# Performance work log

Hardware: AMD Instinct MI355X
Metric: run time of the kernel (lower is better)

## Reference

```python
import jax, jax.numpy as jnp
import numpy as np

GS = 128          # r_group_size
Q_MAX = 7.0       # 2**(q_bits-1)-1, q_bits=4
R_MAX = 7.0       # 2**(r_bits-1)-1, r_bits=4
R_MIN = -8.0      # -R_MAX-1
EPS = 1e-8


def _fake_quant_group(w, n_bits=4, group_size=128, eps=1e-8):
    # symmetric group-wise fake quant of the weight (done once at __init__)
    qmax = 2 ** (n_bits - 1) - 1
    qmin = -qmax - 1
    O, I = w.shape
    wg = w.reshape(O, I // group_size, group_size)
    scale = jnp.maximum(jnp.max(jnp.abs(wg), axis=-1, keepdims=True) / qmax, eps)
    wq = jnp.clip(jnp.round(wg / scale), qmin, qmax) * scale
    return wq.reshape(O, I)


def _select_pow2_base(t):
    # smallest value in {2,4,8,16,32,64} that is >= t (64 if none)
    base = jnp.full_like(t, 64.0)
    for v in (32.0, 16.0, 8.0, 4.0, 2.0):
        base = jnp.where(t <= v, jnp.full_like(t, v), base)
    return base


def setup_inputs() -> dict:
    key = jax.random.key(0)
    kx, kw, kb = jax.random.split(key, 3)
    B, S, IN, OUT = 4, 2048, 4096, 11008
    x = jax.random.normal(kx, (B, S, IN), dtype=jnp.float32)
    w_raw = jax.random.normal(kw, (OUT, IN), dtype=jnp.float32)
    weight = _fake_quant_group(w_raw, n_bits=4, group_size=128)
    bias = jax.random.normal(kb, (OUT,), dtype=jnp.float32)
    return {"x": x, "weight": weight, "bias": bias}


def reference(x, weight, bias):
    # dynamic quotient-remainder activation fake-quant (init path)
    H = x.shape[-1]
    xg = x.astype(jnp.float32).reshape(x.shape[:-1] + (H // GS, GS))  # [..., G, gs]
    max_abs = jnp.maximum(jnp.max(jnp.abs(xg), axis=-1, keepdims=True), EPS)
    base = _select_pow2_base(max_abs / Q_MAX)                 # [..., G, 1]
    q = jnp.clip(jnp.round(xg / base), -Q_MAX, Q_MAX)          # quotient
    r = xg - base * q                                          # remainder
    max_abs_r = jnp.maximum(jnp.max(jnp.abs(r), axis=-1, keepdims=True), EPS)
    scale_r = max_abs_r / R_MAX
    r_dq = jnp.clip(jnp.round(r / scale_r), R_MIN, R_MAX) * scale_r
    x_recon = (base * q + r_dq).reshape(x.shape)
    # F.linear: y = x @ W^T + b
    return jnp.einsum("bsi,oi->bso", x_recon, weight) + bias
```

## Files before the change

kernel.cpp:

```cpp
#include <hip/hip_runtime.h>
#include <stdint.h>
#include <stddef.h>

typedef __bf16 bf16x8 __attribute__((ext_vector_type(8)));
typedef float  f32x4  __attribute__((ext_vector_type(4)));
typedef float  f32x2  __attribute__((ext_vector_type(2)));

__device__ __forceinline__ unsigned short f2bf(float f) {
  unsigned int u = __builtin_bit_cast(unsigned int, f);
  u += 0x7fffu + ((u >> 16) & 1u);
  return (unsigned short)(u >> 16);
}

__device__ __forceinline__ void gld_lds16(const void* g, void* l) {
  __builtin_amdgcn_global_load_lds(
      (__attribute__((address_space(1))) void*)(g),
      (__attribute__((address_space(3))) void*)(l), 16, 0, 0);
}

#define BAR()     asm volatile("s_barrier" ::: "memory")
#define WAITVM(n) asm volatile("s_waitcnt vmcnt(" #n ")" ::: "memory")
#define SCHED0()  __builtin_amdgcn_sched_barrier(0)

__global__ __launch_bounds__(256) void quant_x_kernel(
    const float* __restrict__ x, unsigned short* __restrict__ xb, long long ngroups)
{
  const int lane = threadIdx.x & 63;
  const int wv   = threadIdx.x >> 6;
  long long g = (long long)blockIdx.x * 4 + wv;
  if (g >= ngroups) return;

  const float* xg = x + g * 128;
  f32x2 v = __builtin_nontemporal_load(
      reinterpret_cast<const f32x2*>(xg + lane * 2));

  float m = fmaxf(fabsf(v[0]), fabsf(v[1]));
  #pragma unroll
  for (int off = 32; off; off >>= 1) m = fmaxf(m, __shfl_xor(m, off));
  m = fmaxf(m, 1e-8f);

  float t = m / 7.0f;
  float base = t <= 2.f ? 2.f : t <= 4.f ? 4.f : t <= 8.f ? 8.f
             : t <= 16.f ? 16.f : t <= 32.f ? 32.f : 64.f;
  float inv_base = 1.0f / base;

  float q0 = fminf(fmaxf(rintf(v[0] * inv_base), -7.f), 7.f);
  float q1 = fminf(fmaxf(rintf(v[1] * inv_base), -7.f), 7.f);
  float r0 = v[0] - base * q0;
  float r1 = v[1] - base * q1;

  float mr = fmaxf(fabsf(r0), fabsf(r1));
  #pragma unroll
  for (int off = 32; off; off >>= 1) mr = fmaxf(mr, __shfl_xor(mr, off));
  mr = fmaxf(mr, 1e-8f);
  float scale_r = mr / 7.0f;

  float rd0 = fminf(fmaxf(rintf(r0 / scale_r), -8.f), 7.f) * scale_r;
  float rd1 = fminf(fmaxf(rintf(r1 / scale_r), -8.f), 7.f) * scale_r;

  float y0 = base * q0 + rd0;
  float y1 = base * q1 + rd1;

  unsigned int packed = (unsigned int)f2bf(y0) | ((unsigned int)f2bf(y1) << 16);
  *reinterpret_cast<unsigned int*>(xb + g * 128 + lane * 2) = packed;
}

__global__ __launch_bounds__(256) void cvt_w_kernel(
    const float* __restrict__ w, unsigned short* __restrict__ wb, long long n)
{
  long long i = ((long long)blockIdx.x * blockDim.x + threadIdx.x) * 8;
  if (i + 7 >= n) {
    if (i >= n) return;
    for (long long j = i; j < n; ++j) wb[j] = f2bf(w[j]);
    return;
  }
  f32x4 v0 = __builtin_nontemporal_load(reinterpret_cast<const f32x4*>(w + i));
  f32x4 v1 = __builtin_nontemporal_load(reinterpret_cast<const f32x4*>(w + i + 4));
  uint4 o;
  o.x = (unsigned)f2bf(v0[0]) | ((unsigned)f2bf(v0[1]) << 16);
  o.y = (unsigned)f2bf(v0[2]) | ((unsigned)f2bf(v0[3]) << 16);
  o.z = (unsigned)f2bf(v1[0]) | ((unsigned)f2bf(v1[1]) << 16);
  o.w = (unsigned)f2bf(v1[2]) | ((unsigned)f2bf(v1[3]) << 16);
  *reinterpret_cast<uint4*>(wb + i) = o;
}

#define BM 256
#define BN 256
#define BK 64

#define MFMA16(a, b, c) __builtin_amdgcn_mfma_f32_16x16x32_bf16(a, b, c, 0, 0, 0)

__global__ __launch_bounds__(512, 2) void gemm256_bias(
    const unsigned short* __restrict__ A,
    const unsigned short* __restrict__ B,
    const float* __restrict__ bias,
    float* __restrict__ C,
    int M, int N, int K)
{
  __shared__ unsigned short lds[2][2][2][128 * 64];

  const int tid  = threadIdx.x;
  const int lane = tid & 63;
  const int wid  = tid >> 6;
  const int wm   = wid >> 2;
  const int wn   = wid & 3;
  const int laneq = lane & 15;
  const int laneh = lane >> 4;
  const int lq7   = laneq & 7;

  const int ntm = M / BM;
  const int ntn = N / BN;
  int tm, tn;
  if ((ntm & 15) == 0) {
    int rem = blockIdx.x;
    int str = 0, stc = 0, w = 16;
    for (;;) {
      int w2 = (ntn - stc * 16 < 16) ? (ntn - stc * 16) : 16;
      int sz = 16 * w2;
      if (rem < sz) { w = w2; break; }
      rem -= sz;
      ++stc;
      if (stc * 16 >= ntn) { stc = 0; ++str; }
    }
    if (w == 16) {
      int x = rem & 7, q = rem >> 3;
      tm = str * 16 + 2 * (q & 7) + (x & 1);
      tn = stc * 16 + 4 * (q >> 3) + (x >> 1);
    } else {
      tm = str * 16 + rem / w;
      tn = stc * 16 + rem % w;
    }
  } else {
    tm = (int)blockIdx.x / ntn;
    tn = (int)blockIdx.x % ntn;
  }
  const size_t m0 = (size_t)tm * BM;
  const size_t n0 = (size_t)tn * BN;

  const int NT = K / BK;

  const int ss0 = (laneh ^ lq7);
  const int ss1 = ((4 + laneh) ^ lq7);

  const char* ldsb = (const char*)&lds[0][0][0][0];
  const int aOff = wm * 16384 + laneq * 128;
  const int bOff = 32768 + (wn >> 1) * 16384 + ((wn & 1) * 64 + laneq) * 128;

  const int c0 = tid, c1 = 512 + tid;
  const int r0 = c0 >> 3, sl0 = (c0 & 7) ^ (r0 & 7);
  const int r1 = c1 >> 3, sl1 = (c1 & 7) ^ (r1 & 7);
  const unsigned short* gA0 = A + (m0 + r0) * (size_t)K + sl0 * 8;
  const unsigned short* gA1 = A + (m0 + r1) * (size_t)K + sl1 * 8;
  const unsigned short* gB0 = B + (n0 + r0) * (size_t)K + sl0 * 8;
  const unsigned short* gB1 = B + (n0 + r1) * (size_t)K + sl1 * 8;
  const size_t hstep = (size_t)128 * K;

  char* dst0 = (char*)ldsb + wid * 1024;
  char* dst1 = dst0 + 65536;

  f32x4 acc[8][4];
  #pragma unroll
  for (int i = 0; i < 8; i++)
    #pragma unroll
    for (int j = 0; j < 4; j++)
      acc[i][j] = (f32x4){0.f, 0.f, 0.f, 0.f};

  #define STAGETILE(kt, dstD)                                                \
    do {                                                                     \
      gld_lds16(gA0 + (size_t)(kt) * 64,          (dstD));                   \
      gld_lds16(gA1 + (size_t)(kt) * 64,          (dstD) + 8192);            \
      gld_lds16(gA0 + hstep + (size_t)(kt) * 64,  (dstD) + 16384);           \
      gld_lds16(gA1 + hstep + (size_t)(kt) * 64,  (dstD) + 16384 + 8192);    \
      gld_lds16(gB0 + (size_t)(kt) * 64,          (dstD) + 32768);           \
      gld_lds16(gB1 + (size_t)(kt) * 64,          (dstD) + 32768 + 8192);    \
      gld_lds16(gB0 + hstep + (size_t)(kt) * 64,  (dstD) + 49152);           \
      gld_lds16(gB1 + hstep + (size_t)(kt) * 64,  (dstD) + 49152 + 8192);    \
    } while (0)

  STAGETILE(0, dst0);
  WAITVM(0);
  BAR();

  bf16x8 al[4][2], ah[4][2], bl[2][2], bh[2][2];

  for (int t = 0; t < NT; ++t) {
    const int d = t & 1;
    const char* aS0 = ldsb + (d << 16) + aOff + ss0 * 16;
    const char* aS1 = ldsb + (d << 16) + aOff + ss1 * 16;
    const char* bS0 = ldsb + (d << 16) + bOff + ss0 * 16;
    const char* bS1 = ldsb + (d << 16) + bOff + ss1 * 16;

    if (t + 1 < NT) { char* dn = d ? dst0 : dst1; STAGETILE(t + 1, dn); }

    #pragma unroll
    for (int mi = 0; mi < 4; ++mi) {
      al[mi][0] = *(const bf16x8*)(aS0 + mi * 2048);
      al[mi][1] = *(const bf16x8*)(aS1 + mi * 2048);
    }
    #pragma unroll
    for (int nj = 0; nj < 2; ++nj) {
      bl[nj][0] = *(const bf16x8*)(bS0 + nj * 2048);
      bl[nj][1] = *(const bf16x8*)(bS1 + nj * 2048);
    }
    #pragma unroll
    for (int nj = 0; nj < 2; ++nj) {
      bh[nj][0] = *(const bf16x8*)(bS0 + 4096 + nj * 2048);
      bh[nj][1] = *(const bf16x8*)(bS1 + 4096 + nj * 2048);
    }
    #pragma unroll
    for (int mi = 0; mi < 4; ++mi) {
      ah[mi][0] = *(const bf16x8*)(aS0 + 8192 + mi * 2048);
      ah[mi][1] = *(const bf16x8*)(aS1 + 8192 + mi * 2048);
    }
    SCHED0();

    __builtin_amdgcn_s_setprio(1);
    #pragma unroll
    for (int mi = 0; mi < 4; ++mi)
      #pragma unroll
      for (int nj = 0; nj < 2; ++nj) {
        acc[mi][nj] = MFMA16(al[mi][0], bl[nj][0], acc[mi][nj]);
        acc[mi][nj] = MFMA16(al[mi][1], bl[nj][1], acc[mi][nj]);
      }
    SCHED0();
    #pragma unroll
    for (int mi = 0; mi < 4; ++mi)
      #pragma unroll
      for (int nj = 0; nj < 2; ++nj) {
        acc[mi][2 + nj] = MFMA16(al[mi][0], bh[nj][0], acc[mi][2 + nj]);
        acc[mi][2 + nj] = MFMA16(al[mi][1], bh[nj][1], acc[mi][2 + nj]);
      }
    SCHED0();
    #pragma unroll
    for (int mi = 0; mi < 4; ++mi)
      #pragma unroll
      for (int nj = 0; nj < 2; ++nj) {
        acc[4 + mi][2 + nj] = MFMA16(ah[mi][0], bh[nj][0], acc[4 + mi][2 + nj]);
        acc[4 + mi][2 + nj] = MFMA16(ah[mi][1], bh[nj][1], acc[4 + mi][2 + nj]);
      }
    #pragma unroll
    for (int mi = 0; mi < 4; ++mi)
      #pragma unroll
      for (int nj = 0; nj < 2; ++nj) {
        acc[4 + mi][nj] = MFMA16(ah[mi][0], bl[nj][0], acc[4 + mi][nj]);
        acc[4 + mi][nj] = MFMA16(ah[mi][1], bl[nj][1], acc[4 + mi][nj]);
      }
    __builtin_amdgcn_s_setprio(0);

    WAITVM(0);
    BAR();
  }
  #undef STAGETILE

  #pragma unroll
  for (int nj = 0; nj < 4; ++nj) {
    int col = (int)n0 + wn * 64 + nj * 16 + laneq;
    float bv = bias[col];
    #pragma unroll
    for (int mi = 0; mi < 8; ++mi) {
      size_t row = m0 + wm * 128 + mi * 16 + laneh * 4;
      float* cp = C + row * (size_t)N + col;
      #pragma unroll
      for (int r = 0; r < 4; ++r)
        __builtin_nontemporal_store(acc[mi][nj][r] + bv, cp + (size_t)r * N);
    }
  }
}

extern "C" void kernel_launch(void* const* d_in, const int* in_sizes, int n_in,
                              void* d_out, int out_size, void* d_ws, size_t ws_size,
                              hipStream_t stream) {
  const float* x    = (const float*)d_in[0];
  const float* w    = (const float*)d_in[1];
  const float* bias = (const float*)d_in[2];
  float* out = (float*)d_out;

  const long long xN = in_sizes[0];
  const long long wN = in_sizes[1];
  const int N = in_sizes[2];
  const int K = (int)(wN / N);
  const int M = (int)(xN / K);

  unsigned short* xb = (unsigned short*)d_ws;
  unsigned short* wb = xb + xN;

  long long ngroups = xN / 128;
  long long qblocks = (ngroups + 3) / 4;
  quant_x_kernel<<<(int)qblocks, 256, 0, stream>>>(x, xb, ngroups);

  long long cblocks = (wN + 2047) / 2048;
  cvt_w_kernel<<<(int)cblocks, 256, 0, stream>>>(w, wb, wN);

  int grid = (M / BM) * (N / BN);
  gemm256_bias<<<grid, 512, 0, stream>>>(xb, wb, bias, out, M, N, K);
}
```

Baseline: 755.2 us.

## Split GEMM tile staging into quarter loads interleaved with MFMA phases

Reorganizes the LDS layout into four 128x64 quarter tiles (A low/high, B low/high) and replaces the single whole-tile prefetch with per-quarter global-to-LDS loads. Each load is issued between MFMA phases, and A-low/B-low are prefetched two iterations ahead into the same buffer once they have been consumed. The aim is to spread memory traffic across the iteration and hide load latency behind compute instead of waiting on a full-tile vmcnt(0) at the end of each step. The cost is extra barriers and lgkm waits per iteration, and the cross-buffer reuse depends on the barrier placement being correct.

```diff
diff --git a/kernel.cpp b/kernel.cpp
--- a/kernel.cpp
+++ b/kernel.cpp
@@ -20,6 +20,8 @@
 
 #define BAR()     asm volatile("s_barrier" ::: "memory")
 #define WAITVM(n) asm volatile("s_waitcnt vmcnt(" #n ")" ::: "memory")
+#define LGKM0()   asm volatile("s_waitcnt lgkmcnt(0)" ::: "memory")
+#define LGKM8()   asm volatile("s_waitcnt lgkmcnt(8)" ::: "memory")
 #define SCHED0()  __builtin_amdgcn_sched_barrier(0)
 
 __global__ __launch_bounds__(256) void quant_x_kernel(
@@ -97,7 +99,7 @@
     float* __restrict__ C,
     int M, int N, int K)
 {
-  __shared__ unsigned short lds[2][2][2][128 * 64];
+  __shared__ unsigned short lds[2][4][128 * 64];
 
   const int tid  = threadIdx.x;
   const int lane = tid & 63;
@@ -139,24 +141,39 @@
 
   const int NT = K / BK;
 
-  const int ss0 = (laneh ^ lq7);
-  const int ss1 = ((4 + laneh) ^ lq7);
-
-  const char* ldsb = (const char*)&lds[0][0][0][0];
-  const int aOff = wm * 16384 + laneq * 128;
-  const int bOff = 32768 + (wn >> 1) * 16384 + ((wn & 1) * 64 + laneq) * 128;
-
-  const int c0 = tid, c1 = 512 + tid;
-  const int r0 = c0 >> 3, sl0 = (c0 & 7) ^ (r0 & 7);
-  const int r1 = c1 >> 3, sl1 = (c1 & 7) ^ (r1 & 7);
-  const unsigned short* gA0 = A + (m0 + r0) * (size_t)K + sl0 * 8;
-  const unsigned short* gA1 = A + (m0 + r1) * (size_t)K + sl1 * 8;
-  const unsigned short* gB0 = B + (n0 + r0) * (size_t)K + sl0 * 8;
-  const unsigned short* gB1 = B + (n0 + r1) * (size_t)K + sl1 * 8;
-  const size_t hstep = (size_t)128 * K;
-
-  char* dst0 = (char*)ldsb + wid * 1024;
-  char* dst1 = dst0 + 65536;
+  const int ss0 = (laneh ^ lq7) * 16;
+  const int ss1 = (((4 + laneh) ^ lq7) & 7) * 16;
+
+  const char* ldsb = (const char*)&lds[0][0][0];
+  const int alOff = wm * 8192 + laneq * 128;
+  const int ahOff = 16384 + wm * 8192 + laneq * 128;
+  const int blOff = 32768 + wn * 4096 + laneq * 128;
+  const int bhOff = 49152 + wn * 4096 + laneq * 128;
+
+  const int rA = tid >> 3;
+  const int gs = (tid & 7) ^ ((tid >> 3) & 7);
+  const int rB = (tid >> 8) * 64 + ((tid >> 3) & 31);
+  const unsigned short* gAL = A + (m0 + rA) * (size_t)K + gs * 8;
+  const unsigned short* gAH = A + (m0 + 64 + rA) * (size_t)K + gs * 8;
+  const unsigned short* gBL = B + (n0 + rB) * (size_t)K + gs * 8;
+  const unsigned short* gBH = B + (n0 + 32 + rB) * (size_t)K + gs * 8;
+  const size_t hK = (size_t)128 * K;
+
+  char* db0 = (char*)ldsb;
+  char* db1 = db0 + 65536;
+
+  #define ST_AL(kt, dD) do { \
+      gld_lds16(gAL + (size_t)(kt) * 64,      (dD) + tid * 16);               \
+      gld_lds16(gAL + hK + (size_t)(kt) * 64, (dD) + tid * 16 + 8192); } while (0)
+  #define ST_AH(kt, dD) do { \
+      gld_lds16(gAH + (size_t)(kt) * 64,      (dD) + 16384 + tid * 16);       \
+      gld_lds16(gAH + hK + (size_t)(kt) * 64, (dD) + 16384 + tid * 16 + 8192); } while (0)
+  #define ST_BL(kt, dD) do { \
+      gld_lds16(gBL + (size_t)(kt) * 64,      (dD) + 32768 + tid * 16);       \
+      gld_lds16(gBL + hK + (size_t)(kt) * 64, (dD) + 32768 + tid * 16 + 8192); } while (0)
+  #define ST_BH(kt, dD) do { \
+      gld_lds16(gBH + (size_t)(kt) * 64,      (dD) + 49152 + tid * 16);       \
+      gld_lds16(gBH + hK + (size_t)(kt) * 64, (dD) + 49152 + tid * 16 + 8192); } while (0)
 
   f32x4 acc[8][4];
   #pragma unroll
@@ -165,55 +182,32 @@
     for (int j = 0; j < 4; j++)
       acc[i][j] = (f32x4){0.f, 0.f, 0.f, 0.f};
 
-  #define STAGETILE(kt, dstD)                                                \
-    do {                                                                     \
-      gld_lds16(gA0 + (size_t)(kt) * 64,          (dstD));                   \
-      gld_lds16(gA1 + (size_t)(kt) * 64,          (dstD) + 8192);            \
-      gld_lds16(gA0 + hstep + (size_t)(kt) * 64,  (dstD) + 16384);           \
-      gld_lds16(gA1 + hstep + (size_t)(kt) * 64,  (dstD) + 16384 + 8192);    \
-      gld_lds16(gB0 + (size_t)(kt) * 64,          (dstD) + 32768);           \
-      gld_lds16(gB1 + (size_t)(kt) * 64,          (dstD) + 32768 + 8192);    \
-      gld_lds16(gB0 + hstep + (size_t)(kt) * 64,  (dstD) + 49152);           \
-      gld_lds16(gB1 + hstep + (size_t)(kt) * 64,  (dstD) + 49152 + 8192);    \
-    } while (0)
-
-  STAGETILE(0, dst0);
-  WAITVM(0);
+  ST_AL(0, db0); ST_BL(0, db0); ST_BH(0, db0); ST_AH(0, db0);
+  ST_AL(1, db1); ST_BL(1, db1);
+  WAITVM(4);
   BAR();
 
   bf16x8 al[4][2], ah[4][2], bl[2][2], bh[2][2];
 
   for (int t = 0; t < NT; ++t) {
     const int d = t & 1;
-    const char* aS0 = ldsb + (d << 16) + aOff + ss0 * 16;
-    const char* aS1 = ldsb + (d << 16) + aOff + ss1 * 16;
-    const char* bS0 = ldsb + (d << 16) + bOff + ss0 * 16;
-    const char* bS1 = ldsb + (d << 16) + bOff + ss1 * 16;
-
-    if (t + 1 < NT) { char* dn = d ? dst0 : dst1; STAGETILE(t + 1, dn); }
+    const char* rb = ldsb + (d << 16);
+    char* dOth = d ? db0 : db1;
+    char* dSam = d ? db1 : db0;
 
     #pragma unroll
     for (int mi = 0; mi < 4; ++mi) {
-      al[mi][0] = *(const bf16x8*)(aS0 + mi * 2048);
-      al[mi][1] = *(const bf16x8*)(aS1 + mi * 2048);
+      al[mi][0] = *(const bf16x8*)(rb + alOff + mi * 2048 + ss0);
+      al[mi][1] = *(const bf16x8*)(rb + alOff + mi * 2048 + ss1);
     }
     #pragma unroll
     for (int nj = 0; nj < 2; ++nj) {
-      bl[nj][0] = *(const bf16x8*)(bS0 + nj * 2048);
-      bl[nj][1] = *(const bf16x8*)(bS1 + nj * 2048);
-    }
-    #pragma unroll
-    for (int nj = 0; nj < 2; ++nj) {
-      bh[nj][0] = *(const bf16x8*)(bS0 + 4096 + nj * 2048);
-      bh[nj][1] = *(const bf16x8*)(bS1 + 4096 + nj * 2048);
-    }
-    #pragma unroll
-    for (int mi = 0; mi < 4; ++mi) {
-      ah[mi][0] = *(const bf16x8*)(aS0 + 8192 + mi * 2048);
-      ah[mi][1] = *(const bf16x8*)(aS1 + 8192 + mi * 2048);
-    }
-    SCHED0();
-
+      bl[nj][0] = *(const bf16x8*)(rb + blOff + nj * 2048 + ss0);
+      bl[nj][1] = *(const bf16x8*)(rb + blOff + nj * 2048 + ss1);
+    }
+    if (t + 1 < NT) ST_BH(t + 1, dOth);
+    LGKM8();
+    BAR(); LGKM0(); SCHED0();
     __builtin_amdgcn_s_setprio(1);
     #pragma unroll
     for (int mi = 0; mi < 4; ++mi)
@@ -222,7 +216,17 @@
         acc[mi][nj] = MFMA16(al[mi][0], bl[nj][0], acc[mi][nj]);
         acc[mi][nj] = MFMA16(al[mi][1], bl[nj][1], acc[mi][nj]);
       }
-    SCHED0();
+    __builtin_amdgcn_s_setprio(0);
+    SCHED0(); BAR();
+
+    #pragma unroll
+    for (int nj = 0; nj < 2; ++nj) {
+      bh[nj][0] = *(const bf16x8*)(rb + bhOff + nj * 2048 + ss0);
+      bh[nj][1] = *(const bf16x8*)(rb + bhOff + nj * 2048 + ss1);
+    }
+    if (t + 1 < NT) ST_AH(t + 1, dOth);
+    BAR(); LGKM0(); SCHED0();
+    __builtin_amdgcn_s_setprio(1);
     #pragma unroll
     for (int mi = 0; mi < 4; ++mi)
       #pragma unroll
@@ -230,7 +234,17 @@
         acc[mi][2 + nj] = MFMA16(al[mi][0], bh[nj][0], acc[mi][2 + nj]);
         acc[mi][2 + nj] = MFMA16(al[mi][1], bh[nj][1], acc[mi][2 + nj]);
       }
-    SCHED0();
+    __builtin_amdgcn_s_setprio(0);
+    SCHED0(); BAR();
+
+    #pragma unroll
+    for (int mi = 0; mi < 4; ++mi) {
+      ah[mi][0] = *(const bf16x8*)(rb + ahOff + mi * 2048 + ss0);
+      ah[mi][1] = *(const bf16x8*)(rb + ahOff + mi * 2048 + ss1);
+    }
+    if (t + 2 < NT) ST_AL(t + 2, dSam);
+    BAR(); LGKM0(); SCHED0();
+    __builtin_amdgcn_s_setprio(1);
     #pragma unroll
     for (int mi = 0; mi < 4; ++mi)
       #pragma unroll
@@ -238,6 +252,12 @@
         acc[4 + mi][2 + nj] = MFMA16(ah[mi][0], bh[nj][0], acc[4 + mi][2 + nj]);
         acc[4 + mi][2 + nj] = MFMA16(ah[mi][1], bh[nj][1], acc[4 + mi][2 + nj]);
       }
+    __builtin_amdgcn_s_setprio(0);
+    SCHED0(); BAR();
+
+    if (t + 2 < NT) ST_BL(t + 2, dSam);
+    SCHED0();
+    __builtin_amdgcn_s_setprio(1);
     #pragma unroll
     for (int mi = 0; mi < 4; ++mi)
       #pragma unroll
@@ -246,11 +266,15 @@
         acc[4 + mi][nj] = MFMA16(ah[mi][1], bl[nj][1], acc[4 + mi][nj]);
       }
     __builtin_amdgcn_s_setprio(0);
-
-    WAITVM(0);
+    SCHED0();
+    if (t >= NT - 2) { WAITVM(0); }
+    else             { WAITVM(4); }
     BAR();
   }
-  #undef STAGETILE
+  #undef ST_AL
+  #undef ST_AH
+  #undef ST_BL
+  #undef ST_BH
 
   #pragma unroll
   for (int nj = 0; nj < 4; ++nj) {
```

New measurement: 796.1 us. 5.4% more time.
